# Kernel tuning notes

Hardware: AMD Instinct MI355X
Metric: run time of the kernel (lower is better)

The kernel has to match this reference:

```python
import jax, jax.numpy as jnp
import numpy as np

D_IN = 64   # T (condition_length)
D = 128     # latent_dim
H = 8       # num_head
N = 2       # batch of graphs
M = 512     # num_nodes
T_OBS = 5.0


def leaky(v):
    return jnp.where(v >= 0, v, 0.2 * v)


def setup_inputs() -> dict:
    key = jax.random.key(0)
    ks = jax.random.split(key, 24)
    g = lambda k, s: jax.random.normal(k, s, dtype=jnp.float32) * 0.05
    return {
        "x": jax.random.normal(ks[0], (N, M, D_IN), dtype=jnp.float32),
        # f_node: T -> 2D -> D
        "fn_w1": g(ks[1], (D_IN, 2 * D)), "fn_b1": g(ks[2], (2 * D,)),
        "fn_w2": g(ks[3], (2 * D, D)),   "fn_b2": g(ks[4], (D,)),
        # per-head K/Q/V projections, stacked over heads
        "wk": g(ks[5], (H, D, D)), "bk": g(ks[6], (H, D)),
        "wq": g(ks[7], (H, D, D)), "bq": g(ks[8], (H, D)),
        "wv": g(ks[9], (H, D, D)), "bv": g(ks[10], (H, D)),
        # f_v: H*D -> D -> D
        "fv_w1": g(ks[11], (H * D, D)), "fv_b1": g(ks[12], (D,)),
        "fv_w2": g(ks[13], (D, D)),     "fv_b2": g(ks[14], (D,)),
        # f_node2edge: 2D -> D -> 1
        "fe_w1": g(ks[15], (2 * D, D)), "fe_b1": g(ks[16], (D,)),
        "fe_w2": g(ks[17], (D, 1)),     "fe_b2": g(ks[18], (1,)),
    }


def reference(x, fn_w1, fn_b1, fn_w2, fn_b2, wk, bk, wq, bq, wv, bv,
              fv_w1, fv_b1, fv_w2, fv_b2, fe_w1, fe_b1, fe_w2, fe_b2):
    n, m, T = x.shape
    # TemporalEncoding with d_hid=1: div_term = [1.0], even col -> sin(t)
    t = jnp.linspace(0.0, T_OBS, T)
    te = jnp.sin(t)  # [T]
    # f_node
    h = jax.nn.relu((x + te) @ fn_w1 + fn_b1) @ fn_w2 + fn_b2  # [N,M,D]
    # per-head attention (sender=K_i, receiver=Q_j -> scores = K Q^T)
    K = jnp.einsum('nmd,hde->hnme', h, wk) + bk[:, None, None, :]
    Q = jnp.einsum('nmd,hde->hnme', h, wq) + bq[:, None, None, :]
    V = jnp.einsum('nmd,hde->hnme', h, wv) + bv[:, None, None, :]
    scores = jnp.einsum('hnid,hnjd->hnij', K, Q)           # [H,N,M,M]
    alpha = jax.nn.softmax(leaky(scores), axis=-1)
    att = leaky(jnp.einsum('hnij,hnjd->hnid', alpha, V))   # [H,N,M,D]
    # concat heads along feature dim (head 0 first)
    att = jnp.transpose(att, (1, 2, 0, 3)).reshape(n, m, -1)  # [N,M,H*D]
    x2 = jax.nn.relu(att @ fv_w1 + fv_b1) @ fv_w2 + fv_b2 + h  # [N,M,D]
    # pairwise node2edge FFN: pair(i,j) = concat(x2_i, x2_j)
    half = fe_w1.shape[0] // 2
    A = x2 @ fe_w1[:half]   # contribution of node i
    B = x2 @ fe_w1[half:]   # contribution of node j
    hid = jax.nn.relu(A[:, :, None, :] + B[:, None, :, :] + fe_b1)  # [N,M,M,D]
    edge = (hid @ fe_w2 + fe_b2)[..., 0] / float(m)  # [N,M,M]
    return (x2, edge)
```

## Files before the change

### kernel.cpp

```cpp
#include <hip/hip_runtime.h>

typedef unsigned short u16;
typedef unsigned int u32;
typedef __attribute__((ext_vector_type(8))) short short8;
typedef __attribute__((ext_vector_type(4))) float f32x4;

__device__ __forceinline__ u16 f2b(float f) {
  union { float f; u32 i; } v; v.f = f;
  u32 i = v.i;
  return (u16)((i + 0x7FFFu + ((i >> 16) & 1u)) >> 16);
}
__device__ __forceinline__ float lo16(u32 x) { union { u32 i; float f; } v; v.i = x << 16; return v.f; }
__device__ __forceinline__ float hi16(u32 x) { union { u32 i; float f; } v; v.i = x & 0xffff0000u; return v.f; }
__device__ __forceinline__ u32 pack2(float a, float b) { return (u32)f2b(a) | ((u32)f2b(b) << 16); }

__device__ __align__(16) float g_h[1024 * 128];
__device__ __align__(16) u16   g_hb[1024 * 128];
__device__ __align__(16) u16   g_Wt[24 * 128 * 128];
__device__ __align__(16) u16   g_w1t[128 * 1024];
__device__ __align__(16) u16   g_K[16 * 512 * 128];
__device__ __align__(16) u16   g_Q[16 * 512 * 128];
__device__ __align__(16) u16   g_V[16 * 512 * 128];
__device__ __align__(16) u16   g_Opb[512 * 64 * 128];
__device__ __align__(16) float g_ml[512 * 64 * 2];
__device__ __align__(16) float g_part8[8 * 1024 * 128];
__device__ __align__(16) float g_A[1024 * 128];
__device__ __align__(16) float g_Bm[1024 * 128];

__global__ void k_fnode(const float* __restrict__ x, const float* __restrict__ w1,
                        const float* __restrict__ b1, const float* __restrict__ w2,
                        const float* __restrict__ b2, const float* __restrict__ wk,
                        const float* __restrict__ wq, const float* __restrict__ wv,
                        const float* __restrict__ fvw1) {
  __shared__ float xr[2 * 64];
  __shared__ float hids[2 * 256];
  __shared__ float red[2048];
  int tx = threadIdx.x;
  int row0 = blockIdx.x * 2;
  if (tx < 128) {
    int r = tx >> 6, k = tx & 63;
    xr[tx] = x[(row0 + r) * 64 + k] + sinf((float)k * (5.0f / 63.0f));
  }
  {
    int base = blockIdx.x * 1024 + tx;
#pragma unroll
    for (int t = 0; t < 4; t++) {
      int idx = base + t * 256;
      if (idx < 393216) {
        int ph = idx >> 14, rem = idx & 16383, e = rem >> 7, d = rem & 127;
        int proj = ph >> 3, head = ph & 7;
        const float* W = (proj == 0) ? wk : (proj == 1) ? wq : wv;
        g_Wt[idx] = f2b(W[head * 16384 + d * 128 + e]);
      } else {
        int idx2 = idx - 393216;
        int e = idx2 >> 10, k = idx2 & 1023;
        g_w1t[idx2] = f2b(fvw1[k * 128 + e]);
      }
    }
  }
  __syncthreads();
  {
    int ks = tx >> 6, cg = tx & 63;
    float acc[2][4] = {};
#pragma unroll 4
    for (int i = 0; i < 16; i++) {
      int k = ks * 16 + i;
      float4 w4 = *(const float4*)&w1[k * 256 + cg * 4];
      float a0 = xr[k], a1 = xr[64 + k];
      acc[0][0] = fmaf(a0, w4.x, acc[0][0]); acc[0][1] = fmaf(a0, w4.y, acc[0][1]);
      acc[0][2] = fmaf(a0, w4.z, acc[0][2]); acc[0][3] = fmaf(a0, w4.w, acc[0][3]);
      acc[1][0] = fmaf(a1, w4.x, acc[1][0]); acc[1][1] = fmaf(a1, w4.y, acc[1][1]);
      acc[1][2] = fmaf(a1, w4.z, acc[1][2]); acc[1][3] = fmaf(a1, w4.w, acc[1][3]);
    }
#pragma unroll
    for (int r = 0; r < 2; r++)
      *(float4*)&red[ks * 512 + r * 256 + cg * 4] = *(float4*)acc[r];
  }
  __syncthreads();
#pragma unroll
  for (int jo = 0; jo < 2; jo++) {
    int o = jo * 256 + tx;
    float s = red[o] + red[512 + o] + red[1024 + o] + red[1536 + o];
    hids[o] = fmaxf(s + b1[o & 255], 0.0f);
  }
  __syncthreads();
  {
    int ks = tx >> 5, eg = tx & 31;
    float acc[2][4] = {};
#pragma unroll 4
    for (int i = 0; i < 32; i++) {
      int k = ks * 32 + i;
      float4 w4 = *(const float4*)&w2[k * 128 + eg * 4];
      float a0 = hids[k], a1 = hids[256 + k];
      acc[0][0] = fmaf(a0, w4.x, acc[0][0]); acc[0][1] = fmaf(a0, w4.y, acc[0][1]);
      acc[0][2] = fmaf(a0, w4.z, acc[0][2]); acc[0][3] = fmaf(a0, w4.w, acc[0][3]);
      acc[1][0] = fmaf(a1, w4.x, acc[1][0]); acc[1][1] = fmaf(a1, w4.y, acc[1][1]);
      acc[1][2] = fmaf(a1, w4.z, acc[1][2]); acc[1][3] = fmaf(a1, w4.w, acc[1][3]);
    }
    __syncthreads();
#pragma unroll
    for (int r = 0; r < 2; r++)
      *(float4*)&red[ks * 256 + r * 128 + eg * 4] = *(float4*)acc[r];
  }
  __syncthreads();
  {
    float s = 0.0f;
#pragma unroll
    for (int ks = 0; ks < 8; ks++) s += red[ks * 256 + tx];
    int r = tx >> 7, e = tx & 127;
    float v = s + b2[e];
    g_h[(row0 + r) * 128 + e] = v;
    g_hb[(row0 + r) * 128 + e] = f2b(v);
  }
}

__global__ __launch_bounds__(256) void k_kqv(
    const float* __restrict__ bk, const float* __restrict__ bq,
    const float* __restrict__ bv) {
  __shared__ u16 hs[64 * 136];
  __shared__ u16 Wt[128 * 136];
  int b = blockIdx.x, tx = threadIdx.x;
  int rt = b & 15, ph = b >> 4;
  int proj = ph >> 3, head = ph & 7;
  const float* Bb = (proj == 0) ? bk : (proj == 1) ? bq : bv;
  u16* O = (proj == 0) ? g_K : (proj == 1) ? g_Q : g_V;
  int r0 = rt * 64;
#pragma unroll
  for (int t = 0; t < 4; t++) {
    int idx = t * 256 + tx, row = idx >> 4, oct = idx & 15;
    *(uint4*)&hs[row * 136 + oct * 8] = *(const uint4*)&g_hb[(r0 + row) * 128 + oct * 8];
  }
  const u16* Wtg = g_Wt + ph * 16384;
#pragma unroll
  for (int t = 0; t < 8; t++) {
    int idx = t * 256 + tx, row = idx >> 4, oct = idx & 15;
    *(uint4*)&Wt[row * 136 + oct * 8] = *(const uint4*)&Wtg[row * 128 + oct * 8];
  }
  __syncthreads();
  int lane = tx & 63, wv_ = tx >> 6, cl = lane & 15, quad = lane >> 4;
  short8 bH[4];
#pragma unroll
  for (int kk = 0; kk < 4; kk++)
    bH[kk] = *(const short8*)&hs[(wv_ * 16 + cl) * 136 + kk * 32 + quad * 8];
  f32x4 zero = {0.0f, 0.0f, 0.0f, 0.0f};
  f32x4 acc[8];
#pragma unroll
  for (int em = 0; em < 8; em++) acc[em] = zero;
#pragma unroll
  for (int em = 0; em < 8; em++)
#pragma unroll
    for (int kk = 0; kk < 4; kk++) {
      short8 aW = *(const short8*)&Wt[(em * 16 + cl) * 136 + kk * 32 + quad * 8];
      acc[em] = __builtin_amdgcn_mfma_f32_16x16x32_bf16(aW, bH[kk], acc[em], 0, 0, 0);
    }
#pragma unroll
  for (int em = 0; em < 8; em++) {
    float4 b4 = *(const float4*)&Bb[head * 128 + em * 16 + quad * 4];
    uint2 st = make_uint2(pack2(acc[em][0] + b4.x, acc[em][1] + b4.y),
                          pack2(acc[em][2] + b4.z, acc[em][3] + b4.w));
    *(uint2*)&O[(head * 1024 + r0 + wv_ * 16 + cl) * 128 + em * 16 + quad * 4] = st;
  }
}

__global__ __launch_bounds__(256) void k_attn() {
  __shared__ u16 Ks[64 * 136];
  __shared__ u16 Qs[64 * 136];
  __shared__ u16 Vt[128 * 72];
  __shared__ u16 Pw[4 * 16 * 72];
  __shared__ float alphas[4 * 16];
  int b = blockIdx.x, tx = threadIdx.x;
  int jc = b & 3, it = (b >> 2) & 7, hn = b >> 5;
  int i0 = it * 64;
  const u16* Kp = g_K + hn * 65536;
  const u16* Qp = g_Q + hn * 65536;
  const u16* Vp = g_V + hn * 65536;
#pragma unroll
  for (int t = 0; t < 4; t++) {
    int idx = t * 256 + tx, row = idx >> 4, oct = idx & 15;
    *(uint4*)&Ks[row * 136 + oct * 8] = *(const uint4*)&Kp[(i0 + row) * 128 + oct * 8];
  }
  int lane = tx & 63, wv = tx >> 6;
  int cl = lane & 15, quad = lane >> 4;
  f32x4 zero = {0.0f, 0.0f, 0.0f, 0.0f};
  f32x4 o[8];
#pragma unroll
  for (int es = 0; es < 8; es++) o[es] = zero;
  float m_ = -1e30f, l_ = 0.0f;

  for (int jt = 0; jt < 2; jt++) {
    int j0 = jc * 128 + jt * 64;
    __syncthreads();
#pragma unroll
    for (int t = 0; t < 4; t++) {
      int idx = t * 256 + tx, row = idx >> 4, oct = idx & 15;
      *(uint4*)&Qs[row * 136 + oct * 8] = *(const uint4*)&Qp[(j0 + row) * 128 + oct * 8];
    }
    {
      int jg = (tx & 15) * 4, e8 = (tx >> 4) * 8;
      uint4 r0 = *(const uint4*)&Vp[(j0 + jg + 0) * 128 + e8];
      uint4 r1 = *(const uint4*)&Vp[(j0 + jg + 1) * 128 + e8];
      uint4 r2 = *(const uint4*)&Vp[(j0 + jg + 2) * 128 + e8];
      uint4 r3 = *(const uint4*)&Vp[(j0 + jg + 3) * 128 + e8];
      const u32* p0 = (const u32*)&r0; const u32* p1 = (const u32*)&r1;
      const u32* p2 = (const u32*)&r2; const u32* p3 = (const u32*)&r3;
#pragma unroll
      for (int c = 0; c < 8; c++) {
        int w = c >> 1, sh = (c & 1) * 16;
        u32 lo = ((p0[w] >> sh) & 0xffffu) | (((p1[w] >> sh) & 0xffffu) << 16);
        u32 hi = ((p2[w] >> sh) & 0xffffu) | (((p3[w] >> sh) & 0xffffu) << 16);
        *(uint2*)&Vt[(e8 + c) * 72 + jg] = make_uint2(lo, hi);
      }
    }
    __syncthreads();
    short8 bK[4];
#pragma unroll
    for (int kk = 0; kk < 4; kk++)
      bK[kk] = *(const short8*)&Ks[(wv * 16 + cl) * 136 + kk * 32 + quad * 8];
    f32x4 st[4];
#pragma unroll
    for (int s = 0; s < 4; s++) {
      f32x4 acc = zero;
#pragma unroll
      for (int kk = 0; kk < 4; kk++) {
        short8 aQ = *(const short8*)&Qs[(s * 16 + cl) * 136 + kk * 32 + quad * 8];
        acc = __builtin_amdgcn_mfma_f32_16x16x32_bf16(aQ, bK[kk], acc, 0, 0, 0);
      }
      st[s] = acc;
    }
    float p[4][4];
    float tm = -1e30f;
#pragma unroll
    for (int s = 0; s < 4; s++)
#pragma unroll
      for (int r = 0; r < 4; r++) {
        float v = st[s][r];
        v = fmaxf(v, 0.2f * v);
        p[s][r] = v;
        tm = fmaxf(tm, v);
      }
    tm = fmaxf(tm, __shfl_xor(tm, 16));
    tm = fmaxf(tm, __shfl_xor(tm, 32));
    float mn = fmaxf(m_, tm);
    float alpha = __expf(m_ - mn);
    m_ = mn;
    float ps = 0.0f;
#pragma unroll
    for (int s = 0; s < 4; s++)
#pragma unroll
      for (int r = 0; r < 4; r++) {
        float e = __expf(p[s][r] - mn);
        p[s][r] = e;
        ps += e;
      }
    ps += __shfl_xor(ps, 16);
    ps += __shfl_xor(ps, 32);
    l_ = l_ * alpha + ps;
#pragma unroll
    for (int s = 0; s < 4; s++) {
      uint2 w2v = make_uint2(pack2(p[s][0], p[s][1]), pack2(p[s][2], p[s][3]));
      *(uint2*)&Pw[(wv * 16 + cl) * 72 + s * 16 + quad * 4] = w2v;
    }
    if (quad == 0) alphas[wv * 16 + cl] = alpha;
    __syncthreads();
    f32x4 av = *(const f32x4*)&alphas[wv * 16 + quad * 4];
#pragma unroll
    for (int es = 0; es < 8; es++) o[es] *= av;
    short8 aP[2];
#pragma unroll
    for (int k2 = 0; k2 < 2; k2++)
      aP[k2] = *(const short8*)&Pw[(wv * 16 + cl) * 72 + k2 * 32 + quad * 8];
#pragma unroll
    for (int es = 0; es < 8; es++) {
#pragma unroll
      for (int k2 = 0; k2 < 2; k2++) {
        short8 bV = *(const short8*)&Vt[(es * 16 + cl) * 72 + k2 * 32 + quad * 8];
        o[es] = __builtin_amdgcn_mfma_f32_16x16x32_bf16(aP[k2], bV, o[es], 0, 0, 0);
      }
    }
  }
#pragma unroll
  for (int es = 0; es < 8; es++)
#pragma unroll
    for (int r = 0; r < 4; r++)
      g_Opb[(b * 64 + wv * 16 + quad * 4 + r) * 128 + es * 16 + cl] = f2b(o[es][r]);
  if (quad == 0) {
    g_ml[(b * 64 + wv * 16 + cl) * 2 + 0] = m_;
    g_ml[(b * 64 + wv * 16 + cl) * 2 + 1] = l_;
  }
}

__global__ __launch_bounds__(256) void k_fv1() {
  __shared__ u16 atts[64 * 136];
  __shared__ u16 w1t[128 * 136];
  int b = blockIdx.x, tx = threadIdx.x;
  int kc = b & 7, rt = b >> 3;
  int r0 = rt * 64, k0 = kc * 128;
  int hn = kc * 2 + (rt >> 3), it = rt & 7;
#pragma unroll
  for (int t = 0; t < 8; t++) {
    int idx = t * 256 + tx, row = idx >> 4, oct = idx & 15;
    *(uint4*)&w1t[row * 136 + oct * 8] = *(const uint4*)&g_w1t[row * 1024 + k0 + oct * 8];
  }
  {
    int row = tx >> 2, cs = (tx & 3) * 32;
    float mc[4], lc[4];
#pragma unroll
    for (int c = 0; c < 4; c++) {
      float2 ml = *(const float2*)&g_ml[((hn * 32 + it * 4 + c) * 64 + row) * 2];
      mc[c] = ml.x; lc[c] = ml.y;
    }
    float ms = fmaxf(fmaxf(mc[0], mc[1]), fmaxf(mc[2], mc[3]));
    float lsum = 0.0f;
    float ra[32];
#pragma unroll
    for (int i = 0; i < 32; i++) ra[i] = 0.0f;
#pragma unroll
    for (int c = 0; c < 4; c++) {
      float w = __expf(mc[c] - ms);
      lsum += w * lc[c];
      const u16* src = &g_Opb[((hn * 32 + it * 4 + c) * 64 + row) * 128 + cs];
#pragma unroll
      for (int ov = 0; ov < 4; ov++) {
        uint4 v = *(const uint4*)&src[ov * 8];
        ra[ov * 8 + 0] = fmaf(w, lo16(v.x), ra[ov * 8 + 0]);
        ra[ov * 8 + 1] = fmaf(w, hi16(v.x), ra[ov * 8 + 1]);
        ra[ov * 8 + 2] = fmaf(w, lo16(v.y), ra[ov * 8 + 2]);
        ra[ov * 8 + 3] = fmaf(w, hi16(v.y), ra[ov * 8 + 3]);
        ra[ov * 8 + 4] = fmaf(w, lo16(v.z), ra[ov * 8 + 4]);
        ra[ov * 8 + 5] = fmaf(w, hi16(v.z), ra[ov * 8 + 5]);
        ra[ov * 8 + 6] = fmaf(w, lo16(v.w), ra[ov * 8 + 6]);
        ra[ov * 8 + 7] = fmaf(w, hi16(v.w), ra[ov * 8 + 7]);
      }
    }
    float inv = 1.0f / lsum;
    u32 pk[16];
#pragma unroll
    for (int i = 0; i < 16; i++) {
      float v0 = ra[i * 2] * inv;     v0 = fmaxf(v0, 0.2f * v0);
      float v1 = ra[i * 2 + 1] * inv; v1 = fmaxf(v1, 0.2f * v1);
      pk[i] = pack2(v0, v1);
    }
#pragma unroll
    for (int ov = 0; ov < 4; ov++)
      *(uint4*)&atts[row * 136 + cs + ov * 8] =
          make_uint4(pk[ov * 4], pk[ov * 4 + 1], pk[ov * 4 + 2], pk[ov * 4 + 3]);
  }
  __syncthreads();
  int lane = tx & 63, wv_ = tx >> 6, cl = lane & 15, quad = lane >> 4;
  short8 bA[4];
#pragma unroll
  for (int kk = 0; kk < 4; kk++)
    bA[kk] = *(const short8*)&atts[(wv_ * 16 + cl) * 136 + kk * 32 + quad * 8];
  f32x4 zero = {0.0f, 0.0f, 0.0f, 0.0f};
  f32x4 acc[8];
#pragma unroll
  for (int em = 0; em < 8; em++) acc[em] = zero;
#pragma unroll
  for (int em = 0; em < 8; em++)
#pragma unroll
    for (int kk = 0; kk < 4; kk++) {
      short8 aW = *(const short8*)&w1t[(em * 16 + cl) * 136 + kk * 32 + quad * 8];
      acc[em] = __builtin_amdgcn_mfma_f32_16x16x32_bf16(aW, bA[kk], acc[em], 0, 0, 0);
    }
#pragma unroll
  for (int em = 0; em < 8; em++)
    *(f32x4*)&g_part8[kc * 131072 + (r0 + wv_ * 16 + cl) * 128 + em * 16 + quad * 4] =
        acc[em];
}

__global__ void k_fv2(const float* __restrict__ b1, const float* __restrict__ w2,
                      const float* __restrict__ b2, const float* __restrict__ few1,
                      const float* __restrict__ feb1, float* __restrict__ x2out) {
  __shared__ float hids[2 * 128];
  __shared__ float x2s[2 * 128];
  __shared__ float red[8 * 256];
  int b = blockIdx.x, tx = threadIdx.x;
  int row0 = b * 2;
  {
    int r = tx >> 7, e = tx & 127;
    int gi = (row0 + r) * 128 + e;
    float s = b1[e];
#pragma unroll
    for (int kc = 0; kc < 8; kc++) s += g_part8[kc * 131072 + gi];
    hids[tx] = fmaxf(s, 0.0f);
  }
  __syncthreads();
  int ks = tx >> 5, eg = tx & 31;
  {
    float acc[2][4] = {};
#pragma unroll 4
    for (int i = 0; i < 16; i++) {
      int k = ks * 16 + i;
      float4 w4 = *(const float4*)&w2[k * 128 + eg * 4];
      float a0 = hids[k], a1 = hids[128 + k];
      acc[0][0] = fmaf(a0, w4.x, acc[0][0]); acc[0][1] = fmaf(a0, w4.y, acc[0][1]);
      acc[0][2] = fmaf(a0, w4.z, acc[0][2]); acc[0][3] = fmaf(a0, w4.w, acc[0][3]);
      acc[1][0] = fmaf(a1, w4.x, acc[1][0]); acc[1][1] = fmaf(a1, w4.y, acc[1][1]);
      acc[1][2] = fmaf(a1, w4.z, acc[1][2]); acc[1][3] = fmaf(a1, w4.w, acc[1][3]);
    }
#pragma unroll
    for (int r = 0; r < 2; r++)
      *(float4*)&red[ks * 256 + r * 128 + eg * 4] = *(float4*)acc[r];
  }
  __syncthreads();
  {
    float s = 0.0f;
#pragma unroll
    for (int k8 = 0; k8 < 8; k8++) s += red[k8 * 256 + tx];
    int r = tx >> 7, e = tx & 127;
    int gi = (row0 + r) * 128 + e;
    float c = s + b2[e] + g_h[gi];
    x2s[tx] = c;
    x2out[gi] = c;
  }
  __syncthreads();
  float aA[2][4] = {}, aB[2][4] = {};
#pragma unroll 4
  for (int i = 0; i < 16; i++) {
    int k = ks * 16 + i;
    float4 wa = *(const float4*)&few1[k * 128 + eg * 4];
    float4 wb = *(const float4*)&few1[(128 + k) * 128 + eg * 4];
    float a0 = x2s[k], a1 = x2s[128 + k];
    aA[0][0] = fmaf(a0, wa.x, aA[0][0]); aA[0][1] = fmaf(a0, wa.y, aA[0][1]);
    aA[0][2] = fmaf(a0, wa.z, aA[0][2]); aA[0][3] = fmaf(a0, wa.w, aA[0][3]);
    aA[1][0] = fmaf(a1, wa.x, aA[1][0]); aA[1][1] = fmaf(a1, wa.y, aA[1][1]);
    aA[1][2] = fmaf(a1, wa.z, aA[1][2]); aA[1][3] = fmaf(a1, wa.w, aA[1][3]);
    aB[0][0] = fmaf(a0, wb.x, aB[0][0]); aB[0][1] = fmaf(a0, wb.y, aB[0][1]);
    aB[0][2] = fmaf(a0, wb.z, aB[0][2]); aB[0][3] = fmaf(a0, wb.w, aB[0][3]);
    aB[1][0] = fmaf(a1, wb.x, aB[1][0]); aB[1][1] = fmaf(a1, wb.y, aB[1][1]);
    aB[1][2] = fmaf(a1, wb.z, aB[1][2]); aB[1][3] = fmaf(a1, wb.w, aB[1][3]);
  }
  __syncthreads();
#pragma unroll
  for (int r = 0; r < 2; r++)
    *(float4*)&red[ks * 256 + r * 128 + eg * 4] = *(float4*)aA[r];
  __syncthreads();
  {
    float s = 0.0f;
#pragma unroll
    for (int k8 = 0; k8 < 8; k8++) s += red[k8 * 256 + tx];
    int r = tx >> 7, e = tx & 127;
    g_A[(row0 + r) * 128 + e] = s + feb1[e];
  }
  __syncthreads();
#pragma unroll
  for (int r = 0; r < 2; r++)
    *(float4*)&red[ks * 256 + r * 128 + eg * 4] = *(float4*)aB[r];
  __syncthreads();
  {
    float s = 0.0f;
#pragma unroll
    for (int k8 = 0; k8 < 8; k8++) s += red[k8 * 256 + tx];
    int r = tx >> 7, e = tx & 127;
    g_Bm[(row0 + r) * 128 + e] = s;
  }
}

__global__ void k_edge(const float* __restrict__ few2, const float* __restrict__ feb2,
                       float* __restrict__ edge) {
  __shared__ float As[4 * 128];
  __shared__ float w2s[128];
  int b = blockIdx.x, tx = threadIdx.x;
  int n = b >> 8, rest = b & 255, ig = rest >> 1, jh = rest & 1;
  int i0 = ig * 4;
  if (tx < 128) w2s[tx] = few2[tx];
  As[tx] = g_A[(n * 512 + i0) * 128 + tx];
  As[tx + 256] = g_A[(n * 512 + i0) * 128 + tx + 256];
  float eb2 = feb2[0];
  __syncthreads();
  int j = jh * 256 + tx;
  const float* B0 = &g_Bm[(n * 512 + j) * 128];
  float acc[4] = {};
#pragma unroll 4
  for (int dc = 0; dc < 32; dc++) {
    float4 bv = *(const float4*)&B0[dc * 4];
    float4 w4 = *(const float4*)&w2s[dc * 4];
#pragma unroll
    for (int i = 0; i < 4; i++) {
      float4 a4 = *(const float4*)&As[i * 128 + dc * 4];
      acc[i] = fmaf(fmaxf(a4.x + bv.x, 0.0f), w4.x, acc[i]);
      acc[i] = fmaf(fmaxf(a4.y + bv.y, 0.0f), w4.y, acc[i]);
      acc[i] = fmaf(fmaxf(a4.z + bv.z, 0.0f), w4.z, acc[i]);
      acc[i] = fmaf(fmaxf(a4.w + bv.w, 0.0f), w4.w, acc[i]);
    }
  }
  const float scale = 1.0f / 512.0f;
#pragma unroll
  for (int i = 0; i < 4; i++)
    edge[(n * 512 + i0 + i) * 512 + j] = (acc[i] + eb2) * scale;
}

extern "C" void kernel_launch(void* const* d_in, const int* in_sizes, int n_in,
                              void* d_out, int out_size, void* d_ws, size_t ws_size,
                              hipStream_t stream) {
  (void)in_sizes; (void)n_in; (void)out_size; (void)d_ws; (void)ws_size;
  const float* x     = (const float*)d_in[0];
  const float* fn_w1 = (const float*)d_in[1];
  const float* fn_b1 = (const float*)d_in[2];
  const float* fn_w2 = (const float*)d_in[3];
  const float* fn_b2 = (const float*)d_in[4];
  const float* wk    = (const float*)d_in[5];
  const float* bk    = (const float*)d_in[6];
  const float* wq    = (const float*)d_in[7];
  const float* bq    = (const float*)d_in[8];
  const float* wv    = (const float*)d_in[9];
  const float* bv    = (const float*)d_in[10];
  const float* fv_w1 = (const float*)d_in[11];
  const float* fv_b1 = (const float*)d_in[12];
  const float* fv_w2 = (const float*)d_in[13];
  const float* fv_b2 = (const float*)d_in[14];
  const float* fe_w1 = (const float*)d_in[15];
  const float* fe_b1 = (const float*)d_in[16];
  const float* fe_w2 = (const float*)d_in[17];
  const float* fe_b2 = (const float*)d_in[18];

  float* x2out = (float*)d_out;
  float* edge  = x2out + 131072;

  k_fnode<<<512, 256, 0, stream>>>(x, fn_w1, fn_b1, fn_w2, fn_b2, wk, wq, wv, fv_w1);
  k_kqv<<<384, 256, 0, stream>>>(bk, bq, bv);
  k_attn<<<512, 256, 0, stream>>>();
  k_fv1<<<128, 256, 0, stream>>>();
  k_fv2<<<512, 256, 0, stream>>>(fv_b1, fv_w2, fv_b2, fe_w1, fe_b1, x2out);
  k_edge<<<512, 256, 0, stream>>>(fe_w2, fe_b2, edge);
}
```

Before: 143.1 us.

## Fuse fv1/fv2 into single MFMA kernel removing split-K partial buffer

Merges the head-combine plus fv_w1 GEMM, the fv_w2 GEMM, residual add and the fe_w1 A/B projections into one kernel that works on 16 rows per block. The remaining fp32 scalar GEMMs become bf16 MFMA, with their weights pre-transposed into bf16 in k_fnode. This drops one launch and the 8-way split-K g_part8 round trip through global memory. In exchange the grid shrinks to 64 blocks, each looping serially over 8 K-chunks of reloaded weights, which leaves most CUs idle. Using bf16 for the later GEMMs also lowers precision.

```diff
diff --git a/kernel.cpp b/kernel.cpp
--- a/kernel.cpp
+++ b/kernel.cpp
@@ -18,12 +18,13 @@
 __device__ __align__(16) u16   g_hb[1024 * 128];
 __device__ __align__(16) u16   g_Wt[24 * 128 * 128];
 __device__ __align__(16) u16   g_w1t[128 * 1024];
+__device__ __align__(16) u16   g_w2t[128 * 128];
+__device__ __align__(16) u16   g_fat[2 * 128 * 128];
 __device__ __align__(16) u16   g_K[16 * 512 * 128];
 __device__ __align__(16) u16   g_Q[16 * 512 * 128];
 __device__ __align__(16) u16   g_V[16 * 512 * 128];
 __device__ __align__(16) u16   g_Opb[512 * 64 * 128];
 __device__ __align__(16) float g_ml[512 * 64 * 2];
-__device__ __align__(16) float g_part8[8 * 1024 * 128];
 __device__ __align__(16) float g_A[1024 * 128];
 __device__ __align__(16) float g_Bm[1024 * 128];
 
@@ -31,7 +32,8 @@
                         const float* __restrict__ b1, const float* __restrict__ w2,
                         const float* __restrict__ b2, const float* __restrict__ wk,
                         const float* __restrict__ wq, const float* __restrict__ wv,
-                        const float* __restrict__ fvw1) {
+                        const float* __restrict__ fvw1, const float* __restrict__ fvw2,
+                        const float* __restrict__ few1) {
   __shared__ float xr[2 * 64];
   __shared__ float hids[2 * 256];
   __shared__ float red[2048];
@@ -42,19 +44,28 @@
     xr[tx] = x[(row0 + r) * 64 + k] + sinf((float)k * (5.0f / 63.0f));
   }
   {
-    int base = blockIdx.x * 1024 + tx;
-#pragma unroll
-    for (int t = 0; t < 4; t++) {
+    int base = blockIdx.x * 1280 + tx;
+#pragma unroll
+    for (int t = 0; t < 5; t++) {
       int idx = base + t * 256;
       if (idx < 393216) {
         int ph = idx >> 14, rem = idx & 16383, e = rem >> 7, d = rem & 127;
         int proj = ph >> 3, head = ph & 7;
         const float* W = (proj == 0) ? wk : (proj == 1) ? wq : wv;
         g_Wt[idx] = f2b(W[head * 16384 + d * 128 + e]);
-      } else {
+      } else if (idx < 524288) {
         int idx2 = idx - 393216;
         int e = idx2 >> 10, k = idx2 & 1023;
         g_w1t[idx2] = f2b(fvw1[k * 128 + e]);
+      } else if (idx < 540672) {
+        int idx3 = idx - 524288;
+        int e = idx3 >> 7, k = idx3 & 127;
+        g_w2t[idx3] = f2b(fvw2[k * 128 + e]);
+      } else if (idx < 573440) {
+        int idx4 = idx - 540672;
+        int half = idx4 >> 14, rem = idx4 & 16383;
+        int e = rem >> 7, k = rem & 127;
+        g_fat[idx4] = f2b(few1[(half * 128 + k) * 128 + e]);
       }
     }
   }
@@ -289,38 +300,42 @@
   }
 }
 
-__global__ __launch_bounds__(256) void k_fv1() {
-  __shared__ u16 atts[64 * 136];
-  __shared__ u16 w1t[128 * 136];
+__global__ __launch_bounds__(256) void k_fv(
+    const float* __restrict__ fv_b1, const float* __restrict__ fv_b2,
+    const float* __restrict__ fe_b1, float* __restrict__ x2out) {
+  __shared__ u16 atts[16 * 1032];
+  __shared__ u16 wst[128 * 136];
+  __shared__ u16 hidb[16 * 136];
+  __shared__ u16 x2b[16 * 136];
   int b = blockIdx.x, tx = threadIdx.x;
-  int kc = b & 7, rt = b >> 3;
-  int r0 = rt * 64, k0 = kc * 128;
-  int hn = kc * 2 + (rt >> 3), it = rt & 7;
-#pragma unroll
-  for (int t = 0; t < 8; t++) {
-    int idx = t * 256 + tx, row = idx >> 4, oct = idx & 15;
-    *(uint4*)&w1t[row * 136 + oct * 8] = *(const uint4*)&g_w1t[row * 1024 + k0 + oct * 8];
-  }
-  {
-    int row = tx >> 2, cs = (tx & 3) * 32;
+  int r0 = b * 16;
+
+  {
+    int task = tx >> 1, half = tx & 1;
+    int lr = task >> 3, head = task & 7;
+    int gr = r0 + lr;
+    int n = gr >> 9, i = gr & 511;
+    int it = i >> 6, lr64 = i & 63;
+    int hn = head * 2 + n;
+    int mlbase = (hn * 32 + it * 4) * 64 + lr64;
     float mc[4], lc[4];
 #pragma unroll
     for (int c = 0; c < 4; c++) {
-      float2 ml = *(const float2*)&g_ml[((hn * 32 + it * 4 + c) * 64 + row) * 2];
+      float2 ml = *(const float2*)&g_ml[(mlbase + c * 64) * 2];
       mc[c] = ml.x; lc[c] = ml.y;
     }
     float ms = fmaxf(fmaxf(mc[0], mc[1]), fmaxf(mc[2], mc[3]));
     float lsum = 0.0f;
-    float ra[32];
-#pragma unroll
-    for (int i = 0; i < 32; i++) ra[i] = 0.0f;
+    float ra[64];
+#pragma unroll
+    for (int i2 = 0; i2 < 64; i2++) ra[i2] = 0.0f;
 #pragma unroll
     for (int c = 0; c < 4; c++) {
       float w = __expf(mc[c] - ms);
       lsum += w * lc[c];
-      const u16* src = &g_Opb[((hn * 32 + it * 4 + c) * 64 + row) * 128 + cs];
-#pragma unroll
-      for (int ov = 0; ov < 4; ov++) {
+      const u16* src = &g_Opb[(mlbase + c * 64) * 128 + half * 64];
+#pragma unroll
+      for (int ov = 0; ov < 8; ov++) {
         uint4 v = *(const uint4*)&src[ov * 8];
         ra[ov * 8 + 0] = fmaf(w, lo16(v.x), ra[ov * 8 + 0]);
         ra[ov * 8 + 1] = fmaf(w, hi16(v.x), ra[ov * 8 + 1]);
@@ -333,126 +348,149 @@
       }
     }
     float inv = 1.0f / lsum;
-    u32 pk[16];
-#pragma unroll
-    for (int i = 0; i < 16; i++) {
-      float v0 = ra[i * 2] * inv;     v0 = fmaxf(v0, 0.2f * v0);
-      float v1 = ra[i * 2 + 1] * inv; v1 = fmaxf(v1, 0.2f * v1);
-      pk[i] = pack2(v0, v1);
-    }
-#pragma unroll
-    for (int ov = 0; ov < 4; ov++)
-      *(uint4*)&atts[row * 136 + cs + ov * 8] =
+    u32 pk[32];
+#pragma unroll
+    for (int i2 = 0; i2 < 32; i2++) {
+      float v0 = ra[i2 * 2] * inv;     v0 = fmaxf(v0, 0.2f * v0);
+      float v1 = ra[i2 * 2 + 1] * inv; v1 = fmaxf(v1, 0.2f * v1);
+      pk[i2] = pack2(v0, v1);
+    }
+    int dst = lr * 1032 + head * 128 + half * 64;
+#pragma unroll
+    for (int ov = 0; ov < 8; ov++)
+      *(uint4*)&atts[dst + ov * 8] =
           make_uint4(pk[ov * 4], pk[ov * 4 + 1], pk[ov * 4 + 2], pk[ov * 4 + 3]);
   }
   __syncthreads();
-  int lane = tx & 63, wv_ = tx >> 6, cl = lane & 15, quad = lane >> 4;
-  short8 bA[4];
+
+  int lane = tx & 63, w = tx >> 6, cl = lane & 15, quad = lane >> 4;
+  f32x4 zero = {0.0f, 0.0f, 0.0f, 0.0f};
+
+  f32x4 accH[2] = {zero, zero};
+  for (int kc = 0; kc < 8; kc++) {
+#pragma unroll
+    for (int q = 0; q < 8; q++) {
+      int idx = q * 256 + tx, row = idx >> 4, oct = idx & 15;
+      *(uint4*)&wst[row * 136 + oct * 8] =
+          *(const uint4*)&g_w1t[row * 1024 + kc * 128 + oct * 8];
+    }
+    __syncthreads();
+    short8 bA[4];
+#pragma unroll
+    for (int kk = 0; kk < 4; kk++)
+      bA[kk] = *(const short8*)&atts[cl * 1032 + kc * 128 + kk * 32 + quad * 8];
+#pragma unroll
+    for (int t2 = 0; t2 < 2; t2++) {
+      int em = 2 * w + t2;
+#pragma unroll
+      for (int kk = 0; kk < 4; kk++) {
+        short8 aW = *(const short8*)&wst[(em * 16 + cl) * 136 + kk * 32 + quad * 8];
+        accH[t2] = __builtin_amdgcn_mfma_f32_16x16x32_bf16(aW, bA[kk], accH[t2], 0, 0, 0);
+      }
+    }
+    __syncthreads();
+  }
+
+#pragma unroll
+  for (int t2 = 0; t2 < 2; t2++) {
+    int eb = (2 * w + t2) * 16 + quad * 4;
+    float4 b4 = *(const float4*)&fv_b1[eb];
+    float v0 = fmaxf(accH[t2][0] + b4.x, 0.0f);
+    float v1 = fmaxf(accH[t2][1] + b4.y, 0.0f);
+    float v2 = fmaxf(accH[t2][2] + b4.z, 0.0f);
+    float v3 = fmaxf(accH[t2][3] + b4.w, 0.0f);
+    *(u32*)&hidb[cl * 136 + eb] = pack2(v0, v1);
+    *(u32*)&hidb[cl * 136 + eb + 2] = pack2(v2, v3);
+  }
+#pragma unroll
+  for (int q = 0; q < 8; q++) {
+    int idx = q * 256 + tx, row = idx >> 4, oct = idx & 15;
+    *(uint4*)&wst[row * 136 + oct * 8] = *(const uint4*)&g_w2t[row * 128 + oct * 8];
+  }
+  __syncthreads();
+
+  {
+    short8 bH2[4];
+#pragma unroll
+    for (int kk = 0; kk < 4; kk++)
+      bH2[kk] = *(const short8*)&hidb[cl * 136 + kk * 32 + quad * 8];
+    int gr = r0 + cl;
+#pragma unroll
+    for (int t2 = 0; t2 < 2; t2++) {
+      int em = 2 * w + t2;
+      f32x4 acc2 = zero;
+#pragma unroll
+      for (int kk = 0; kk < 4; kk++) {
+        short8 aW = *(const short8*)&wst[(em * 16 + cl) * 136 + kk * 32 + quad * 8];
+        acc2 = __builtin_amdgcn_mfma_f32_16x16x32_bf16(aW, bH2[kk], acc2, 0, 0, 0);
+      }
+      int eb = em * 16 + quad * 4;
+      float4 b4 = *(const float4*)&fv_b2[eb];
+      float4 h4 = *(const float4*)&g_h[gr * 128 + eb];
+      float4 xv;
+      xv.x = acc2[0] + b4.x + h4.x;
+      xv.y = acc2[1] + b4.y + h4.y;
+      xv.z = acc2[2] + b4.z + h4.z;
+      xv.w = acc2[3] + b4.w + h4.w;
+      *(float4*)&x2out[gr * 128 + eb] = xv;
+      *(u32*)&x2b[cl * 136 + eb] = pack2(xv.x, xv.y);
+      *(u32*)&x2b[cl * 136 + eb + 2] = pack2(xv.z, xv.w);
+    }
+  }
+  __syncthreads();
+
+#pragma unroll
+  for (int q = 0; q < 8; q++) {
+    int idx = q * 256 + tx, row = idx >> 4, oct = idx & 15;
+    *(uint4*)&wst[row * 136 + oct * 8] = *(const uint4*)&g_fat[row * 128 + oct * 8];
+  }
+  __syncthreads();
+  short8 bX[4];
 #pragma unroll
   for (int kk = 0; kk < 4; kk++)
-    bA[kk] = *(const short8*)&atts[(wv_ * 16 + cl) * 136 + kk * 32 + quad * 8];
-  f32x4 zero = {0.0f, 0.0f, 0.0f, 0.0f};
-  f32x4 acc[8];
-#pragma unroll
-  for (int em = 0; em < 8; em++) acc[em] = zero;
-#pragma unroll
-  for (int em = 0; em < 8; em++)
-#pragma unroll
-    for (int kk = 0; kk < 4; kk++) {
-      short8 aW = *(const short8*)&w1t[(em * 16 + cl) * 136 + kk * 32 + quad * 8];
-      acc[em] = __builtin_amdgcn_mfma_f32_16x16x32_bf16(aW, bA[kk], acc[em], 0, 0, 0);
-    }
-#pragma unroll
-  for (int em = 0; em < 8; em++)
-    *(f32x4*)&g_part8[kc * 131072 + (r0 + wv_ * 16 + cl) * 128 + em * 16 + quad * 4] =
-        acc[em];
-}
-
-__global__ void k_fv2(const float* __restrict__ b1, const float* __restrict__ w2,
-                      const float* __restrict__ b2, const float* __restrict__ few1,
-                      const float* __restrict__ feb1, float* __restrict__ x2out) {
-  __shared__ float hids[2 * 128];
-  __shared__ float x2s[2 * 128];
-  __shared__ float red[8 * 256];
-  int b = blockIdx.x, tx = threadIdx.x;
-  int row0 = b * 2;
-  {
-    int r = tx >> 7, e = tx & 127;
-    int gi = (row0 + r) * 128 + e;
-    float s = b1[e];
-#pragma unroll
-    for (int kc = 0; kc < 8; kc++) s += g_part8[kc * 131072 + gi];
-    hids[tx] = fmaxf(s, 0.0f);
-  }
-  __syncthreads();
-  int ks = tx >> 5, eg = tx & 31;
-  {
-    float acc[2][4] = {};
-#pragma unroll 4
-    for (int i = 0; i < 16; i++) {
-      int k = ks * 16 + i;
-      float4 w4 = *(const float4*)&w2[k * 128 + eg * 4];
-      float a0 = hids[k], a1 = hids[128 + k];
-      acc[0][0] = fmaf(a0, w4.x, acc[0][0]); acc[0][1] = fmaf(a0, w4.y, acc[0][1]);
-      acc[0][2] = fmaf(a0, w4.z, acc[0][2]); acc[0][3] = fmaf(a0, w4.w, acc[0][3]);
-      acc[1][0] = fmaf(a1, w4.x, acc[1][0]); acc[1][1] = fmaf(a1, w4.y, acc[1][1]);
-      acc[1][2] = fmaf(a1, w4.z, acc[1][2]); acc[1][3] = fmaf(a1, w4.w, acc[1][3]);
-    }
-#pragma unroll
-    for (int r = 0; r < 2; r++)
-      *(float4*)&red[ks * 256 + r * 128 + eg * 4] = *(float4*)acc[r];
-  }
-  __syncthreads();
-  {
-    float s = 0.0f;
-#pragma unroll
-    for (int k8 = 0; k8 < 8; k8++) s += red[k8 * 256 + tx];
-    int r = tx >> 7, e = tx & 127;
-    int gi = (row0 + r) * 128 + e;
-    float c = s + b2[e] + g_h[gi];
-    x2s[tx] = c;
-    x2out[gi] = c;
-  }
-  __syncthreads();
-  float aA[2][4] = {}, aB[2][4] = {};
-#pragma unroll 4
-  for (int i = 0; i < 16; i++) {
-    int k = ks * 16 + i;
-    float4 wa = *(const float4*)&few1[k * 128 + eg * 4];
-    float4 wb = *(const float4*)&few1[(128 + k) * 128 + eg * 4];
-    float a0 = x2s[k], a1 = x2s[128 + k];
-    aA[0][0] = fmaf(a0, wa.x, aA[0][0]); aA[0][1] = fmaf(a0, wa.y, aA[0][1]);
-    aA[0][2] = fmaf(a0, wa.z, aA[0][2]); aA[0][3] = fmaf(a0, wa.w, aA[0][3]);
-    aA[1][0] = fmaf(a1, wa.x, aA[1][0]); aA[1][1] = fmaf(a1, wa.y, aA[1][1]);
-    aA[1][2] = fmaf(a1, wa.z, aA[1][2]); aA[1][3] = fmaf(a1, wa.w, aA[1][3]);
-    aB[0][0] = fmaf(a0, wb.x, aB[0][0]); aB[0][1] = fmaf(a0, wb.y, aB[0][1]);
-    aB[0][2] = fmaf(a0, wb.z, aB[0][2]); aB[0][3] = fmaf(a0, wb.w, aB[0][3]);
-    aB[1][0] = fmaf(a1, wb.x, aB[1][0]); aB[1][1] = fmaf(a1, wb.y, aB[1][1]);
-    aB[1][2] = fmaf(a1, wb.z, aB[1][2]); aB[1][3] = fmaf(a1, wb.w, aB[1][3]);
-  }
-  __syncthreads();
-#pragma unroll
-  for (int r = 0; r < 2; r++)
-    *(float4*)&red[ks * 256 + r * 128 + eg * 4] = *(float4*)aA[r];
-  __syncthreads();
-  {
-    float s = 0.0f;
-#pragma unroll
-    for (int k8 = 0; k8 < 8; k8++) s += red[k8 * 256 + tx];
-    int r = tx >> 7, e = tx & 127;
-    g_A[(row0 + r) * 128 + e] = s + feb1[e];
-  }
-  __syncthreads();
-#pragma unroll
-  for (int r = 0; r < 2; r++)
-    *(float4*)&red[ks * 256 + r * 128 + eg * 4] = *(float4*)aB[r];
-  __syncthreads();
-  {
-    float s = 0.0f;
-#pragma unroll
-    for (int k8 = 0; k8 < 8; k8++) s += red[k8 * 256 + tx];
-    int r = tx >> 7, e = tx & 127;
-    g_Bm[(row0 + r) * 128 + e] = s;
+    bX[kk] = *(const short8*)&x2b[cl * 136 + kk * 32 + quad * 8];
+  {
+    int gr = r0 + cl;
+#pragma unroll
+    for (int t2 = 0; t2 < 2; t2++) {
+      int em = 2 * w + t2;
+      f32x4 accA = zero;
+#pragma unroll
+      for (int kk = 0; kk < 4; kk++) {
+        short8 aW = *(const short8*)&wst[(em * 16 + cl) * 136 + kk * 32 + quad * 8];
+        accA = __builtin_amdgcn_mfma_f32_16x16x32_bf16(aW, bX[kk], accA, 0, 0, 0);
+      }
+      int eb = em * 16 + quad * 4;
+      float4 b4 = *(const float4*)&fe_b1[eb];
+      float4 av;
+      av.x = accA[0] + b4.x; av.y = accA[1] + b4.y;
+      av.z = accA[2] + b4.z; av.w = accA[3] + b4.w;
+      *(float4*)&g_A[gr * 128 + eb] = av;
+    }
+  }
+  __syncthreads();
+
+#pragma unroll
+  for (int q = 0; q < 8; q++) {
+    int idx = q * 256 + tx, row = idx >> 4, oct = idx & 15;
+    *(uint4*)&wst[row * 136 + oct * 8] =
+        *(const uint4*)&g_fat[16384 + row * 128 + oct * 8];
+  }
+  __syncthreads();
+  {
+    int gr = r0 + cl;
+#pragma unroll
+    for (int t2 = 0; t2 < 2; t2++) {
+      int em = 2 * w + t2;
+      f32x4 accB = zero;
+#pragma unroll
+      for (int kk = 0; kk < 4; kk++) {
+        short8 aW = *(const short8*)&wst[(em * 16 + cl) * 136 + kk * 32 + quad * 8];
+        accB = __builtin_amdgcn_mfma_f32_16x16x32_bf16(aW, bX[kk], accB, 0, 0, 0);
+      }
+      int eb = em * 16 + quad * 4;
+      *(f32x4*)&g_Bm[gr * 128 + eb] = accB;
+    }
   }
 }
 
@@ -517,10 +555,10 @@
   float* x2out = (float*)d_out;
   float* edge  = x2out + 131072;
 
-  k_fnode<<<512, 256, 0, stream>>>(x, fn_w1, fn_b1, fn_w2, fn_b2, wk, wq, wv, fv_w1);
+  k_fnode<<<512, 256, 0, stream>>>(x, fn_w1, fn_b1, fn_w2, fn_b2, wk, wq, wv,
+                                   fv_w1, fv_w2, fe_w1);
   k_kqv<<<384, 256, 0, stream>>>(bk, bq, bv);
   k_attn<<<512, 256, 0, stream>>>();
-  k_fv1<<<128, 256, 0, stream>>>();
-  k_fv2<<<512, 256, 0, stream>>>(fv_b1, fv_w2, fv_b2, fe_w1, fe_b1, x2out);
+  k_fv<<<64, 256, 0, stream>>>(fv_b1, fv_b2, fe_b1, x2out);
   k_edge<<<512, 256, 0, stream>>>(fe_w2, fe_b2, edge);
 }
```

New measurement: 144.1 us. About the same (+0.7%).
